# Performance work log

Hardware: AMD Instinct MI355X
Metric: run time of the kernel (lower is better)

The kernel has to match this reference:

```python
import jax, jax.numpy as jnp
import numpy as np


def setup_inputs() -> dict:
    key = jax.random.key(0)
    k1, k2, k3, k4 = jax.random.split(key, 4)
    B, C_in, C_out, H, W = 8, 256, 256, 160, 160
    mask = jax.random.randint(k1, (B, 1, H, W), 0, 2, dtype=jnp.int32)  # binary hard mask
    ori = jax.random.normal(k2, (B, C_in, H, W), dtype=jnp.float32)
    weight = jax.random.normal(k3, (C_out, C_in, 3, 3), dtype=jnp.float32) * 0.02
    bias = jax.random.normal(k4, (C_out,), dtype=jnp.float32) * 0.02
    return {"mask": mask, "ori": ori, "weight": weight, "bias": bias}


def reference(mask, ori, weight, bias):
    # apply_mask: broadcast binary [B,1,H,W] mask over channels, zero masked regions
    x = ori * mask.astype(ori.dtype)
    # dense 3x3 conv, stride 1, padding 1 (SAME) -> output [B, C_out, H, W]
    out = jax.lax.conv_general_dilated(
        x, weight,
        window_strides=(1, 1),
        padding='SAME',
        dimension_numbers=('NCHW', 'OIHW', 'NCHW'),
    )
    return out + bias[None, :, None, None]
```

## Files before the change

kernel.cpp:

```cpp
#include <hip/hip_runtime.h>

typedef __attribute__((ext_vector_type(8))) short short8;
typedef __attribute__((ext_vector_type(4))) float f32x4;

#define B_    8
#define CI    256
#define CO    256
#define Hh    160
#define Ww    160
#define HP    162
#define WP    162
#define HWp   (Hh * Ww)
#define XPAD_ELEMS (B_ * HP * WP * CI)
#define W3_ELEMS   (9 * CI * CO)
#define NT    36
#define BSLOT (160 * 64)

#define NBORD 644
#define NPW   2304
#define NPX   (B_ * Hh * 4 * 3)

__device__ __forceinline__ unsigned short f2bf(float f) {
  unsigned int u = __float_as_uint(f);
  u += 0x7FFFu + ((u >> 16) & 1u);
  return (unsigned short)(u >> 16);
}

__global__ void prep_all(const float* __restrict__ ori, const int* __restrict__ mask,
                         const float* __restrict__ w,
                         unsigned short* __restrict__ xp, unsigned short* __restrict__ w3) {
  __shared__ float tile[64][65];
  const int bid = blockIdx.x;
  const int t = threadIdx.x;

  if (bid < NBORD) {
    int g = bid * 256 + t;
    int pos = g >> 5;
    int c = (g & 31) << 3;
    int n = pos / 644;
    int p = pos - n * 644;
    int y, x;
    if (p < 324) { y = (p < 162) ? 0 : 161; x = (p < 162) ? p : p - 162; }
    else { int q = p - 324; y = 1 + (q >> 1); x = (q & 1) ? 161 : 0; }
    unsigned short* d = xp + (((size_t)(n * 162 + y)) * 162 + x) * 256 + c;
    *(uint4*)d = (uint4){0u, 0u, 0u, 0u};
    return;
  }
  if (bid < NBORD + NPW) {
    int i = (bid - NBORD) * 256 + t;
    int e = i & 7, l = (i >> 3) & 63, g = i >> 9;
    int mi = g & 1, wm = (g >> 1) & 3, kk = (g >> 3) & 1;
    int qm = (g >> 4) & 1, cic = (g >> 5) & 3, shift = g >> 7;
    int co = qm * 128 + wm * 32 + mi * 16 + (l & 15);
    int ci = cic * 64 + kk * 32 + (l >> 4) * 8 + e;
    w3[i] = f2bf(w[(co * 256 + ci) * 9 + shift]);
    return;
  }

  int bid2 = bid - (NBORD + NPW);
  int wt = bid2 % 3;
  int t1 = bid2 / 3;
  int cit = t1 & 3;
  int t2 = t1 >> 2;
  int h = t2 % Hh;
  int n = t2 / Hh;

  int wl = t & 63;
  int ww = wt * 64 + wl;
  bool valid = (ww < Ww);
  float m = 0.f;
  if (valid) m = (float)mask[(n * Hh + h) * Ww + ww];
  const float* src = ori + (((size_t)(n * CI + cit * 64) * Hh + h) * Ww + ww);
  int r0 = t >> 6;
#pragma unroll
  for (int k = 0; k < 16; ++k) {
    int ci_l = r0 * 16 + k;
    float v = 0.f;
    if (valid) v = src[(size_t)ci_l * HWp] * m;
    tile[ci_l][wl] = v;
  }
  __syncthreads();

  int wl2 = t >> 2;
  int wo = wt * 64 + wl2;
  if (wo < Ww) {
    int cseg = (t & 3) * 16;
    union { unsigned short u[8]; uint4 v; } p0, p1;
#pragma unroll
    for (int j = 0; j < 8; ++j) p0.u[j] = f2bf(tile[cseg + j][wl2]);
#pragma unroll
    for (int j = 0; j < 8; ++j) p1.u[j] = f2bf(tile[cseg + 8 + j][wl2]);
    unsigned short* dst = xp + ((size_t)((n * HP + h + 1) * WP) + (wo + 1)) * CI + cit * 64 + cseg;
    *(uint4*)dst = p0.v;
    *(uint4*)(dst + 8) = p1.v;
  }
}

__device__ __forceinline__ void gload16(const unsigned short* g, unsigned short* l) {
  __builtin_amdgcn_global_load_lds((const __attribute__((address_space(1))) void*)g,
                                   (__attribute__((address_space(3))) void*)l, 16, 0, 0);
}

__global__ void __launch_bounds__(512, 2)
sconv_gemm(const unsigned short* __restrict__ xp, const unsigned short* __restrict__ w3,
           const float* __restrict__ bias, float* __restrict__ out) {
  __shared__ unsigned short Bs[3][BSLOT];

  const int bid = blockIdx.x;
  const int n = bid & 7;
  const int h = bid >> 3;

  const int t = threadIdx.x;
  const int l = t & 63;
  const int wv = t >> 6;
  const int q = wv >> 1;
  const int wn = wv & 1;

  const int lr = l >> 3;
  const int swz8 = ((l & 7) ^ lr) << 3;
  const int lc = l & 15, hi4 = l >> 4, lx7 = l & 7;
  const unsigned xrow = (unsigned)(n * HP + h);

  const unsigned boff0 = (unsigned)(wv * 8 + lr) * 256 + swz8;

  f32x4 acc[4][5];
#pragma unroll
  for (int j = 0; j < 4; ++j)
#pragma unroll
    for (int ni = 0; ni < 5; ++ni)
      acc[j][ni] = (f32x4){0.f, 0.f, 0.f, 0.f};

  short8 aK0[4], aK1[4], bb[5];

#define TPAR(ts, cic, sh, kh, kw)                                             \
  const int cic = ((ts) * 57) >> 9;                                           \
  const int sh = (ts) - cic * 9;                                              \
  const int kh = (sh * 11) >> 5;                                              \
  const int kw = sh - kh * 3;

  auto STG = [&](int ts, unsigned short* slot) {
    TPAR(ts, cic, sh, kh, kw)
    (void)sh;
    const unsigned short* src = xp + ((size_t)(xrow + kh) * WP + kw) * 256 + (cic << 6) + boff0;
    unsigned short* dst = slot + (wv * 8) * 64;
    gload16(src, dst);
    gload16(src + 64 * 256, dst + 64 * 64);
    if (wv < 4) gload16(src + 128 * 256, dst + 128 * 64);
  };

  auto AGH = [&](int ts, int kk, short8* dst) {
    TPAR(ts, cic, sh, kh, kw)
    (void)kh; (void)kw;
    const unsigned short* p = w3 +
        ((size_t)(sh * 128 + cic * 32 + (q >> 1) * 16 + kk * 8 + (q & 1) * 4) << 9) + (l << 3);
#pragma unroll
    for (int j = 0; j < 4; ++j)
      dst[j] = *(const short8*)(p + (j << 9));
  };

#define BBR(slot, kk) do {                                                    \
  _Pragma("unroll")                                                           \
  for (int i = 0; i < 5; ++i)                                                 \
    bb[i] = *(const short8*)((slot) + ((wn * 80 + i * 16 + lc) * 64) +        \
                             (((((kk) << 2) + hi4) ^ lx7) << 3));             \
} while (0)

#define CL(AH) do {                                                           \
  __builtin_amdgcn_s_setprio(1);                                              \
  _Pragma("unroll")                                                           \
  for (int j = 0; j < 4; ++j)                                                 \
    _Pragma("unroll")                                                         \
    for (int i = 0; i < 5; ++i)                                               \
      acc[j][i] = __builtin_amdgcn_mfma_f32_16x16x32_bf16(                    \
          AH[j], bb[i], acc[j][i], 0, 0, 0);                                  \
  __builtin_amdgcn_s_setprio(0);                                              \
} while (0)

#define PH(slot, kk, AH, ISSUES, ENDW) do {                                   \
  ISSUES                                                                      \
  BBR(slot, kk);                                                              \
  __builtin_amdgcn_s_barrier();                                               \
  CL(AH);                                                                     \
  ENDW                                                                        \
  __builtin_amdgcn_s_barrier();                                               \
} while (0)

#define TILEWAIT do {                                                         \
  if (wv < 4) asm volatile("s_waitcnt vmcnt(11)" ::: "memory");               \
  else        asm volatile("s_waitcnt vmcnt(10)" ::: "memory");               \
} while (0)

#define TILE(tt, sc, sn) do {                                                 \
  PH(sc, 0, aK0, { STG((tt) + 2, sn); }, {});                                 \
  PH(sc, 1, aK1, { AGH((tt) + 1, 0, aK0); },                                  \
     { AGH((tt) + 1, 1, aK1); TILEWAIT; });                                   \
} while (0)

  unsigned short* const s0 = &Bs[0][0];
  unsigned short* const s1 = &Bs[1][0];
  unsigned short* const s2 = &Bs[2][0];

  STG(0, s0);
  STG(1, s1);
  AGH(0, 0, aK0);
  AGH(0, 1, aK1);
  asm volatile("s_waitcnt vmcnt(0)" ::: "memory");
  __builtin_amdgcn_s_barrier();

  for (int t3 = 0; t3 < 33; t3 += 3) {
    TILE(t3 + 0, s0, s2);
    TILE(t3 + 1, s1, s0);
    TILE(t3 + 2, s2, s1);
  }
  TILE(33, s0, s2);
  PH(s1, 0, aK0, {}, {});
  PH(s1, 1, aK1, { AGH(35, 0, aK0); },
     { AGH(35, 1, aK1);
       asm volatile("s_waitcnt vmcnt(8)" ::: "memory"); });
  PH(s2, 0, aK0, {}, {});
  {
    BBR(s2, 1);
    CL(aK1);
  }

#pragma unroll
  for (int j = 0; j < 4; ++j) {
    int cobase = q * 64 + j * 16 + hi4 * 4;
    const float4 bv = *(const float4*)(bias + cobase);
    float* op = out + (((size_t)n * CO + cobase) * Hh + h) * Ww;
#pragma unroll
    for (int ni = 0; ni < 5; ++ni) {
      int w = wn * 80 + ni * 16 + lc;
      f32x4 v = acc[j][ni];
      op[w]                   = v[0] + bv.x;
      op[(size_t)HWp + w]     = v[1] + bv.y;
      op[(size_t)2 * HWp + w] = v[2] + bv.z;
      op[(size_t)3 * HWp + w] = v[3] + bv.w;
    }
  }
}

extern "C" void kernel_launch(void* const* d_in, const int* in_sizes, int n_in,
                              void* d_out, int out_size, void* d_ws, size_t ws_size,
                              hipStream_t stream) {
  const int* mask = (const int*)d_in[0];
  const float* ori = (const float*)d_in[1];
  const float* weight = (const float*)d_in[2];
  const float* bias = (const float*)d_in[3];
  float* out = (float*)d_out;

  unsigned short* xp = (unsigned short*)d_ws;
  unsigned short* w3 = xp + XPAD_ELEMS;

  prep_all<<<NBORD + NPW + NPX, 256, 0, stream>>>(ori, mask, weight, xp, w3);
  sconv_gemm<<<1280, 512, 0, stream>>>(xp, w3, bias, out);
}
```

Before: 368.3 us.

## Retile conv GEMM to 128-pixel by 128-channel blocks with 256 threads

The implicit-GEMM conv previously used 512-thread blocks covering one image row of 160 pixels and all 256 output channels. It now uses 256-thread blocks that cover 128 flattened pixels and half of the output channels, with precomputed per-group row offsets so a tile can span row boundaries. Each wave's MFMA tile shrinks from 4x5 to 4x4. The aim is more blocks per CU (launch bounds 3) and better load balance over 3200 blocks, at the cost of loading each input tile twice (once per channel half) and less reuse per block.

```diff
diff --git a/kernel.cpp b/kernel.cpp
--- a/kernel.cpp
+++ b/kernel.cpp
@@ -14,7 +14,7 @@
 #define XPAD_ELEMS (B_ * HP * WP * CI)
 #define W3_ELEMS   (9 * CI * CO)
 #define NT    36
-#define BSLOT (160 * 64)
+#define BSLOT (128 * 64)
 
 #define NBORD 644
 #define NPW   2304
@@ -101,36 +101,45 @@
                                    (__attribute__((address_space(3))) void*)l, 16, 0, 0);
 }
 
-__global__ void __launch_bounds__(512, 2)
+__global__ void __launch_bounds__(256, 3)
 sconv_gemm(const unsigned short* __restrict__ xp, const unsigned short* __restrict__ w3,
            const float* __restrict__ bias, float* __restrict__ out) {
   __shared__ unsigned short Bs[3][BSLOT];
 
   const int bid = blockIdx.x;
   const int n = bid & 7;
-  const int h = bid >> 3;
+  const int rest = bid >> 3;
+  const int ch = rest & 1;
+  const int pxt = rest >> 1;
+  const int p0 = pxt * 128;
 
   const int t = threadIdx.x;
   const int l = t & 63;
   const int wv = t >> 6;
-  const int q = wv >> 1;
+  const int wm = wv >> 1;
   const int wn = wv & 1;
 
   const int lr = l >> 3;
   const int swz8 = ((l & 7) ^ lr) << 3;
   const int lc = l & 15, hi4 = l >> 4, lx7 = l & 7;
-  const unsigned xrow = (unsigned)(n * HP + h);
-
-  const unsigned boff0 = (unsigned)(wv * 8 + lr) * 256 + swz8;
-
-  f32x4 acc[4][5];
+
+  unsigned boff[4];
+#pragma unroll
+  for (int g = 0; g < 4; ++g) {
+    int p = p0 + wv * 32 + g * 8 + lr;
+    int h = p / Ww;
+    int w = p - h * Ww;
+    boff[g] = (unsigned)((n * HP + h) * WP + w) * 256 + swz8;
+  }
+
+  f32x4 acc[4][4];
 #pragma unroll
   for (int j = 0; j < 4; ++j)
 #pragma unroll
-    for (int ni = 0; ni < 5; ++ni)
-      acc[j][ni] = (f32x4){0.f, 0.f, 0.f, 0.f};
-
-  short8 aK0[4], aK1[4], bb[5];
+    for (int i = 0; i < 4; ++i)
+      acc[j][i] = (f32x4){0.f, 0.f, 0.f, 0.f};
+
+  short8 aK0[4], aK1[4], bb[4];
 
 #define TPAR(ts, cic, sh, kh, kw)                                             \
   const int cic = ((ts) * 57) >> 9;                                           \
@@ -141,18 +150,18 @@
   auto STG = [&](int ts, unsigned short* slot) {
     TPAR(ts, cic, sh, kh, kw)
     (void)sh;
-    const unsigned short* src = xp + ((size_t)(xrow + kh) * WP + kw) * 256 + (cic << 6) + boff0;
-    unsigned short* dst = slot + (wv * 8) * 64;
-    gload16(src, dst);
-    gload16(src + 64 * 256, dst + 64 * 64);
-    if (wv < 4) gload16(src + 128 * 256, dst + 128 * 64);
+    const unsigned bd = (unsigned)(kh * WP + kw) * 256 + (cic << 6);
+    unsigned short* dst = slot + wv * 2048;
+#pragma unroll
+    for (int g = 0; g < 4; ++g)
+      gload16(xp + bd + boff[g], dst + g * 512);
   };
 
   auto AGH = [&](int ts, int kk, short8* dst) {
     TPAR(ts, cic, sh, kh, kw)
     (void)kh; (void)kw;
     const unsigned short* p = w3 +
-        ((size_t)(sh * 128 + cic * 32 + (q >> 1) * 16 + kk * 8 + (q & 1) * 4) << 9) + (l << 3);
+        ((size_t)(sh * 128 + cic * 32 + ch * 16 + kk * 8 + wm * 4) << 9) + (l << 3);
 #pragma unroll
     for (int j = 0; j < 4; ++j)
       dst[j] = *(const short8*)(p + (j << 9));
@@ -160,8 +169,8 @@
 
 #define BBR(slot, kk) do {                                                    \
   _Pragma("unroll")                                                           \
-  for (int i = 0; i < 5; ++i)                                                 \
-    bb[i] = *(const short8*)((slot) + ((wn * 80 + i * 16 + lc) * 64) +        \
+  for (int i = 0; i < 4; ++i)                                                 \
+    bb[i] = *(const short8*)((slot) + ((wn * 64 + i * 16 + lc) * 64) +        \
                              (((((kk) << 2) + hi4) ^ lx7) << 3));             \
 } while (0)
 
@@ -170,7 +179,7 @@
   _Pragma("unroll")                                                           \
   for (int j = 0; j < 4; ++j)                                                 \
     _Pragma("unroll")                                                         \
-    for (int i = 0; i < 5; ++i)                                               \
+    for (int i = 0; i < 4; ++i)                                               \
       acc[j][i] = __builtin_amdgcn_mfma_f32_16x16x32_bf16(                    \
           AH[j], bb[i], acc[j][i], 0, 0, 0);                                  \
   __builtin_amdgcn_s_setprio(0);                                              \
@@ -185,15 +194,11 @@
   __builtin_amdgcn_s_barrier();                                               \
 } while (0)
 
-#define TILEWAIT do {                                                         \
-  if (wv < 4) asm volatile("s_waitcnt vmcnt(11)" ::: "memory");               \
-  else        asm volatile("s_waitcnt vmcnt(10)" ::: "memory");               \
-} while (0)
-
 #define TILE(tt, sc, sn) do {                                                 \
   PH(sc, 0, aK0, { STG((tt) + 2, sn); }, {});                                 \
   PH(sc, 1, aK1, { AGH((tt) + 1, 0, aK0); },                                  \
-     { AGH((tt) + 1, 1, aK1); TILEWAIT; });                                   \
+     { AGH((tt) + 1, 1, aK1);                                                 \
+       asm volatile("s_waitcnt vmcnt(12)" ::: "memory"); });                  \
 } while (0)
 
   unsigned short* const s0 = &Bs[0][0];
@@ -204,7 +209,7 @@
   STG(1, s1);
   AGH(0, 0, aK0);
   AGH(0, 1, aK1);
-  asm volatile("s_waitcnt vmcnt(0)" ::: "memory");
+  asm volatile("s_waitcnt vmcnt(12)" ::: "memory");
   __builtin_amdgcn_s_barrier();
 
   for (int t3 = 0; t3 < 33; t3 += 3) {
@@ -225,17 +230,17 @@
 
 #pragma unroll
   for (int j = 0; j < 4; ++j) {
-    int cobase = q * 64 + j * 16 + hi4 * 4;
+    int cobase = ch * 128 + wm * 64 + j * 16 + hi4 * 4;
     const float4 bv = *(const float4*)(bias + cobase);
-    float* op = out + (((size_t)n * CO + cobase) * Hh + h) * Ww;
-#pragma unroll
-    for (int ni = 0; ni < 5; ++ni) {
-      int w = wn * 80 + ni * 16 + lc;
-      f32x4 v = acc[j][ni];
-      op[w]                   = v[0] + bv.x;
-      op[(size_t)HWp + w]     = v[1] + bv.y;
-      op[(size_t)2 * HWp + w] = v[2] + bv.z;
-      op[(size_t)3 * HWp + w] = v[3] + bv.w;
+#pragma unroll
+    for (int i = 0; i < 4; ++i) {
+      int px = p0 + wn * 64 + i * 16 + lc;
+      float* op = out + ((size_t)n * CO + cobase) * HWp + px;
+      f32x4 v = acc[j][i];
+      op[0]               = v[0] + bv.x;
+      op[(size_t)HWp]     = v[1] + bv.y;
+      op[(size_t)2 * HWp] = v[2] + bv.z;
+      op[(size_t)3 * HWp] = v[3] + bv.w;
     }
   }
 }
@@ -253,5 +258,5 @@
   unsigned short* w3 = xp + XPAD_ELEMS;
 
   prep_all<<<NBORD + NPW + NPX, 256, 0, stream>>>(ori, mask, weight, xp, w3);
-  sconv_gemm<<<1280, 512, 0, stream>>>(xp, w3, bias, out);
-}
+  sconv_gemm<<<3200, 256, 0, stream>>>(xp, w3, bias, out);
+}
```

Measured after the change: 339.2 us. -7.9%, faster.

## Retile implicit-GEMM conv to 256x256 tiles with LDS-staged weights

Applied to the files above, without the earlier changes.

Each block now handles 256 output channels by 256 flattened pixels (spanning row boundaries) instead of one image row of 160 pixels, with a 2x4 wave grid computing 128x64 per wave. Weights move from per-wave register loads out of global memory into triple-buffered LDS via global_load_lds, while the pixel operand is double-buffered. The weight prep layout is simplified to plain [shift][co][ci]. The larger tile raises arithmetic intensity and cuts the grid from 1280 to 800 blocks. In exchange it uses more LDS and accumulator registers and a more barrier-heavy four-phase schedule per K step.

```diff
diff --git a/kernel.cpp b/kernel.cpp
--- a/kernel.cpp
+++ b/kernel.cpp
@@ -12,9 +12,10 @@
 #define WP    162
 #define HWp   (Hh * Ww)
 #define XPAD_ELEMS (B_ * HP * WP * CI)
-#define W3_ELEMS   (9 * CI * CO)
+#define W2_ELEMS   (9 * CI * CO)
 #define NT    36
-#define BSLOT (160 * 64)
+#define ASL   16384
+#define BSL   16384
 
 #define NBORD 644
 #define NPW   2304
@@ -28,7 +29,7 @@
 
 __global__ void prep_all(const float* __restrict__ ori, const int* __restrict__ mask,
                          const float* __restrict__ w,
-                         unsigned short* __restrict__ xp, unsigned short* __restrict__ w3) {
+                         unsigned short* __restrict__ xp, unsigned short* __restrict__ w2) {
   __shared__ float tile[64][65];
   const int bid = blockIdx.x;
   const int t = threadIdx.x;
@@ -48,12 +49,11 @@
   }
   if (bid < NBORD + NPW) {
     int i = (bid - NBORD) * 256 + t;
-    int e = i & 7, l = (i >> 3) & 63, g = i >> 9;
-    int mi = g & 1, wm = (g >> 1) & 3, kk = (g >> 3) & 1;
-    int qm = (g >> 4) & 1, cic = (g >> 5) & 3, shift = g >> 7;
-    int co = qm * 128 + wm * 32 + mi * 16 + (l & 15);
-    int ci = cic * 64 + kk * 32 + (l >> 4) * 8 + e;
-    w3[i] = f2bf(w[(co * 256 + ci) * 9 + shift]);
+    int ci = i & 255;
+    int t2 = i >> 8;
+    int co = t2 & 255;
+    int s = t2 >> 8;
+    w2[i] = f2bf(w[(co * 256 + ci) * 9 + s]);
     return;
   }
 
@@ -102,35 +102,49 @@
 }
 
 __global__ void __launch_bounds__(512, 2)
-sconv_gemm(const unsigned short* __restrict__ xp, const unsigned short* __restrict__ w3,
+sconv_gemm(const unsigned short* __restrict__ xp, const unsigned short* __restrict__ w2,
            const float* __restrict__ bias, float* __restrict__ out) {
-  __shared__ unsigned short Bs[3][BSLOT];
+  __shared__ unsigned short As[3 * ASL];
+  __shared__ unsigned short Bs[2 * BSL];
 
   const int bid = blockIdx.x;
   const int n = bid & 7;
-  const int h = bid >> 3;
+  const int pxt = bid >> 3;
+  const int p0 = pxt * 256;
 
   const int t = threadIdx.x;
   const int l = t & 63;
   const int wv = t >> 6;
-  const int q = wv >> 1;
-  const int wn = wv & 1;
+  const int wm = wv >> 2;
+  const int wn = wv & 3;
 
   const int lr = l >> 3;
   const int swz8 = ((l & 7) ^ lr) << 3;
   const int lc = l & 15, hi4 = l >> 4, lx7 = l & 7;
-  const unsigned xrow = (unsigned)(n * HP + h);
-
-  const unsigned boff0 = (unsigned)(wv * 8 + lr) * 256 + swz8;
-
-  f32x4 acc[4][5];
-#pragma unroll
-  for (int j = 0; j < 4; ++j)
-#pragma unroll
-    for (int ni = 0; ni < 5; ++ni)
-      acc[j][ni] = (f32x4){0.f, 0.f, 0.f, 0.f};
-
-  short8 aK0[4], aK1[4], bb[5];
+
+  const unsigned awoff = (unsigned)(wv * 32 + lr) * 256 + swz8;
+  unsigned boffB[4];
+#pragma unroll
+  for (int g = 0; g < 4; ++g) {
+    int p = p0 + wv * 32 + g * 8 + lr;
+    int h = p / Ww;
+    int w = p - h * Ww;
+    boffB[g] = (unsigned)((n * HP + h) * WP + w) * 256 + swz8;
+  }
+
+  const int abase = (wm * 128 + lc) * 64;
+  const int bbase = (wn * 64 + lc) * 64;
+  const int sA0 = ((0 + hi4) ^ lx7) << 3;
+  const int sA1 = ((4 + hi4) ^ lx7) << 3;
+
+  f32x4 acc[8][4];
+#pragma unroll
+  for (int j = 0; j < 8; ++j)
+#pragma unroll
+    for (int i = 0; i < 4; ++i)
+      acc[j][i] = (f32x4){0.f, 0.f, 0.f, 0.f};
+
+  short8 aa[8], bb0[4], bb1[4];
 
 #define TPAR(ts, cic, sh, kh, kw)                                             \
   const int cic = ((ts) * 57) >> 9;                                           \
@@ -138,100 +152,122 @@
   const int kh = (sh * 11) >> 5;                                              \
   const int kw = sh - kh * 3;
 
-  auto STG = [&](int ts, unsigned short* slot) {
-    TPAR(ts, cic, sh, kh, kw)
-    (void)sh;
-    const unsigned short* src = xp + ((size_t)(xrow + kh) * WP + kw) * 256 + (cic << 6) + boff0;
-    unsigned short* dst = slot + (wv * 8) * 64;
-    gload16(src, dst);
-    gload16(src + 64 * 256, dst + 64 * 64);
-    if (wv < 4) gload16(src + 128 * 256, dst + 128 * 64);
-  };
-
-  auto AGH = [&](int ts, int kk, short8* dst) {
-    TPAR(ts, cic, sh, kh, kw)
-    (void)kh; (void)kw;
-    const unsigned short* p = w3 +
-        ((size_t)(sh * 128 + cic * 32 + (q >> 1) * 16 + kk * 8 + (q & 1) * 4) << 9) + (l << 3);
-#pragma unroll
-    for (int j = 0; j < 4; ++j)
-      dst[j] = *(const short8*)(p + (j << 9));
-  };
-
-#define BBR(slot, kk) do {                                                    \
+#define ASTG(ts, SLOT, part) do {                                             \
+  TPAR(ts, cic_, sh_, kh_, kw_) (void)kh_; (void)kw_;                         \
+  const unsigned short* base_ = w2 + sh_ * 65536 + (cic_ << 6) + awoff;       \
+  unsigned short* dst_ = As + (SLOT) * ASL + wv * 2048 + (part) * 1024;       \
+  gload16(base_ + (part) * 4096, dst_);                                       \
+  gload16(base_ + (part) * 4096 + 2048, dst_ + 512);                          \
+} while (0)
+
+#define BSTG(ts, BIDX, part) do {                                             \
+  TPAR(ts, cic_, sh_, kh_, kw_)                                               \
+  const unsigned bd_ = (unsigned)(kh_ * WP + kw_) * 256 + (cic_ << 6);        \
+  unsigned short* dst_ = Bs + (BIDX) * BSL + wv * 2048 + (part) * 1024;       \
+  gload16(xp + bd_ + boffB[(part) * 2], dst_);                                \
+  gload16(xp + bd_ + boffB[(part) * 2 + 1], dst_ + 512);                      \
+} while (0)
+
+#define BBA(mh, AC) do {                                                      \
   _Pragma("unroll")                                                           \
-  for (int i = 0; i < 5; ++i)                                                 \
-    bb[i] = *(const short8*)((slot) + ((wn * 80 + i * 16 + lc) * 64) +        \
-                             (((((kk) << 2) + hi4) ^ lx7) << 3));             \
-} while (0)
-
-#define CL(AH) do {                                                           \
+  for (int mf = 0; mf < 4; ++mf) {                                            \
+    aa[mf]     = *(const short8*)((AC) + abase + ((mh)*4+mf)*1024 + sA0);     \
+    aa[4 + mf] = *(const short8*)((AC) + abase + ((mh)*4+mf)*1024 + sA1);     \
+  }                                                                           \
+} while (0)
+
+#define BBB(nh, bb, BC) do {                                                  \
+  _Pragma("unroll")                                                           \
+  for (int nf = 0; nf < 2; ++nf) {                                            \
+    bb[nf]     = *(const short8*)((BC) + bbase + ((nh)*2+nf)*1024 + sA0);     \
+    bb[2 + nf] = *(const short8*)((BC) + bbase + ((nh)*2+nf)*1024 + sA1);     \
+  }                                                                           \
+} while (0)
+
+#define CL16(mh, nh, bb) do {                                                 \
   __builtin_amdgcn_s_setprio(1);                                              \
   _Pragma("unroll")                                                           \
-  for (int j = 0; j < 4; ++j)                                                 \
+  for (int kk = 0; kk < 2; ++kk)                                              \
     _Pragma("unroll")                                                         \
-    for (int i = 0; i < 5; ++i)                                               \
-      acc[j][i] = __builtin_amdgcn_mfma_f32_16x16x32_bf16(                    \
-          AH[j], bb[i], acc[j][i], 0, 0, 0);                                  \
+    for (int mf = 0; mf < 4; ++mf)                                            \
+      _Pragma("unroll")                                                       \
+      for (int nf = 0; nf < 2; ++nf)                                          \
+        acc[(mh)*4+mf][(nh)*2+nf] = __builtin_amdgcn_mfma_f32_16x16x32_bf16(  \
+            aa[kk*4+mf], bb[kk*2+nf], acc[(mh)*4+mf][(nh)*2+nf], 0, 0, 0);    \
   __builtin_amdgcn_s_setprio(0);                                              \
 } while (0)
 
-#define PH(slot, kk, AH, ISSUES, ENDW) do {                                   \
-  ISSUES                                                                      \
-  BBR(slot, kk);                                                              \
-  __builtin_amdgcn_s_barrier();                                               \
-  CL(AH);                                                                     \
-  ENDW                                                                        \
-  __builtin_amdgcn_s_barrier();                                               \
-} while (0)
-
-#define TILEWAIT do {                                                         \
-  if (wv < 4) asm volatile("s_waitcnt vmcnt(11)" ::: "memory");               \
-  else        asm volatile("s_waitcnt vmcnt(10)" ::: "memory");               \
-} while (0)
-
-#define TILE(tt, sc, sn) do {                                                 \
-  PH(sc, 0, aK0, { STG((tt) + 2, sn); }, {});                                 \
-  PH(sc, 1, aK1, { AGH((tt) + 1, 0, aK0); },                                  \
-     { AGH((tt) + 1, 1, aK1); TILEWAIT; });                                   \
-} while (0)
-
-  unsigned short* const s0 = &Bs[0][0];
-  unsigned short* const s1 = &Bs[1][0];
-  unsigned short* const s2 = &Bs[2][0];
-
-  STG(0, s0);
-  STG(1, s1);
-  AGH(0, 0, aK0);
-  AGH(0, 1, aK1);
+#define BAR __builtin_amdgcn_s_barrier()
+
+#define TILE(tt, TA, TB, SA2, SB1) do {                                       \
+  const unsigned short* Ac = As + (TA) * ASL;                                 \
+  const unsigned short* Bc = Bs + (TB) * BSL;                                 \
+  BSTG((tt) + 1, SB1, 0); BBA(0, Ac); BBB(0, bb0, Bc);                        \
+  BAR; CL16(0, 0, bb0); BAR;                                                  \
+  BSTG((tt) + 1, SB1, 1); BBB(1, bb1, Bc);                                    \
+  BAR; CL16(0, 1, bb1); BAR;                                                  \
+  ASTG((tt) + 2, SA2, 0); BBA(1, Ac);                                         \
+  BAR; CL16(1, 1, bb1); BAR;                                                  \
+  ASTG((tt) + 2, SA2, 1); BBB(0, bb0, Bc);                                    \
+  BAR; CL16(1, 0, bb0);                                                       \
+  asm volatile("s_waitcnt vmcnt(4)" ::: "memory");                            \
+  BAR;                                                                        \
+} while (0)
+
+  ASTG(0, 0, 0); ASTG(0, 0, 1);
+  ASTG(1, 1, 0); ASTG(1, 1, 1);
+  BSTG(0, 0, 0); BSTG(0, 0, 1);
   asm volatile("s_waitcnt vmcnt(0)" ::: "memory");
-  __builtin_amdgcn_s_barrier();
-
-  for (int t3 = 0; t3 < 33; t3 += 3) {
-    TILE(t3 + 0, s0, s2);
-    TILE(t3 + 1, s1, s0);
-    TILE(t3 + 2, s2, s1);
-  }
-  TILE(33, s0, s2);
-  PH(s1, 0, aK0, {}, {});
-  PH(s1, 1, aK1, { AGH(35, 0, aK0); },
-     { AGH(35, 1, aK1);
-       asm volatile("s_waitcnt vmcnt(8)" ::: "memory"); });
-  PH(s2, 0, aK0, {}, {});
+  BAR;
+
+  for (int k6 = 0; k6 < 30; k6 += 6) {
+    TILE(k6 + 0, 0, 0, 2, 1);
+    TILE(k6 + 1, 1, 1, 0, 0);
+    TILE(k6 + 2, 2, 0, 1, 1);
+    TILE(k6 + 3, 0, 1, 2, 0);
+    TILE(k6 + 4, 1, 0, 0, 1);
+    TILE(k6 + 5, 2, 1, 1, 0);
+  }
+  TILE(30, 0, 0, 2, 1);
+  TILE(31, 1, 1, 0, 0);
+  TILE(32, 2, 0, 1, 1);
+  TILE(33, 0, 1, 2, 0);
   {
-    BBR(s2, 1);
-    CL(aK1);
-  }
-
-#pragma unroll
-  for (int j = 0; j < 4; ++j) {
-    int cobase = q * 64 + j * 16 + hi4 * 4;
+    const unsigned short* Ac = As + 1 * ASL;
+    const unsigned short* Bc = Bs + 0 * BSL;
+    BSTG(35, 1, 0); BBA(0, Ac); BBB(0, bb0, Bc);
+    BAR; CL16(0, 0, bb0); BAR;
+    BSTG(35, 1, 1); BBB(1, bb1, Bc);
+    BAR; CL16(0, 1, bb1); BAR;
+    BBA(1, Ac);
+    BAR; CL16(1, 1, bb1); BAR;
+    BBB(0, bb0, Bc);
+    BAR; CL16(1, 0, bb0);
+    asm volatile("s_waitcnt vmcnt(0)" ::: "memory");
+    BAR;
+  }
+  {
+    const unsigned short* Ac = As + 2 * ASL;
+    const unsigned short* Bc = Bs + 1 * BSL;
+    BBA(0, Ac); BBB(0, bb0, Bc);
+    BAR; CL16(0, 0, bb0); BAR;
+    BBB(1, bb1, Bc);
+    BAR; CL16(0, 1, bb1); BAR;
+    BBA(1, Ac);
+    BAR; CL16(1, 1, bb1); BAR;
+    BBB(0, bb0, Bc);
+    CL16(1, 0, bb0);
+  }
+
+#pragma unroll
+  for (int mf = 0; mf < 8; ++mf) {
+    int cobase = wm * 128 + mf * 16 + hi4 * 4;
     const float4 bv = *(const float4*)(bias + cobase);
-    float* op = out + (((size_t)n * CO + cobase) * Hh + h) * Ww;
-#pragma unroll
-    for (int ni = 0; ni < 5; ++ni) {
-      int w = wn * 80 + ni * 16 + lc;
-      f32x4 v = acc[j][ni];
+    float* op = out + ((size_t)n * CO + cobase) * HWp + p0 + wn * 64;
+#pragma unroll
+    for (int nf = 0; nf < 4; ++nf) {
+      int w = nf * 16 + lc;
+      f32x4 v = acc[mf][nf];
       op[w]                   = v[0] + bv.x;
       op[(size_t)HWp + w]     = v[1] + bv.y;
       op[(size_t)2 * HWp + w] = v[2] + bv.z;
@@ -250,8 +286,8 @@
   float* out = (float*)d_out;
 
   unsigned short* xp = (unsigned short*)d_ws;
-  unsigned short* w3 = xp + XPAD_ELEMS;
-
-  prep_all<<<NBORD + NPW + NPX, 256, 0, stream>>>(ori, mask, weight, xp, w3);
-  sconv_gemm<<<1280, 512, 0, stream>>>(xp, w3, bias, out);
-}
+  unsigned short* w2 = xp + XPAD_ELEMS;
+
+  prep_all<<<NBORD + NPW + NPX, 256, 0, stream>>>(ori, mask, weight, xp, w2);
+  sconv_gemm<<<800, 512, 0, stream>>>(xp, w2, bias, out);
+}
```

Result: slower. 425.9 us (+15.6%).
